# Kernel optimization log

Hardware: AMD Instinct MI355X
Metric: run time of the kernel (lower is better)

## Reference

```python
import jax, jax.numpy as jnp
import numpy as np

B, N, K, L = 16, 1024, 5, 3       # batch, atoms, kNN, egnn layers
D, M, H = 16, 64, 64              # embed_dim, m_dim, hidden_dim
EIN = 2 * D + 1                   # edge_mlp input: feats_i | feats_j | rel_dist
EPS, CLAMP = 1e-8, 2.0

def silu(x):
    return x * jax.nn.sigmoid(x)

def egnn_layer(feats, coors, mask, p):
    (eW1, eb1, eW2, eb2, gW, gb, cscale,
     cW1, cb1, cW2, cb2, nW1, nb1, nW2, nb2) = p
    b = feats.shape[0]
    rel_coors = coors[:, :, None, :] - coors[:, None, :, :]              # [B,N,N,3]
    rel_dist = jnp.sum(rel_coors ** 2, axis=-1)                          # [B,N,N] squared dist
    rank_mask = mask[:, :, None] & mask[:, None, :]
    ranking = jnp.where(rank_mask, rel_dist, 1e5)
    _, nbhd_idx = jax.lax.top_k(-ranking, K)                             # k nearest (incl self)
    rel_coors = jnp.take_along_axis(rel_coors, nbhd_idx[..., None], axis=2)   # [B,N,K,3]
    rel_dist = jnp.take_along_axis(rel_dist, nbhd_idx, axis=2)[..., None]     # [B,N,K,1]
    b_idx = jnp.arange(b)[:, None, None]
    feats_j = feats[b_idx, nbhd_idx]                                     # [B,N,K,D]
    feats_i = jnp.broadcast_to(feats[:, :, None, :], feats_j.shape)
    edge_in = jnp.concatenate([feats_i, feats_j, rel_dist], axis=-1)     # [B,N,K,2D+1]
    m_ij = silu(silu(edge_in @ eW1 + eb1) @ eW2 + eb2)                   # [B,N,K,M]
    m_ij = m_ij * jax.nn.sigmoid(m_ij @ gW + gb)                         # soft edge gate
    pair_mask = mask[:, :, None] & mask[b_idx, nbhd_idx]                 # [B,N,K]
    # coordinate update: CoorsNorm (unit vectors * learned scale) + clamped weights
    cw = (silu(m_ij @ cW1 + cb1) @ cW2 + cb2)[..., 0]                    # [B,N,K]
    sq = jnp.sum(rel_coors ** 2, axis=-1, keepdims=True)
    norm = jnp.sqrt(jnp.maximum(sq, EPS * EPS))                          # == norm.clamp(min=eps)
    rel_unit = rel_coors / norm * cscale
    cw = jnp.clip(jnp.where(pair_mask, cw, 0.0), -CLAMP, CLAMP)
    coors_out = jnp.einsum('bnk,bnkc->bnc', cw, rel_unit) + coors
    # node update: masked sum-pool of messages, residual MLP
    m_i = jnp.sum(jnp.where(pair_mask[..., None], m_ij, 0.0), axis=2)    # [B,N,M]
    node_in = jnp.concatenate([feats, m_i], axis=-1)
    feats_out = silu(node_in @ nW1 + nb1) @ nW2 + nb2 + feats
    return feats_out, coors_out

def _forward(atom_types, pos, mask, emb, eW1, eb1, eW2, eb2, gW, gb, cscale,
             cW1, cb1, cW2, cb2, nW1, nb1, nW2, nb2,
             hW1, hb1, hW2, hb2, hW3, hb3):
    maskf = mask.astype(jnp.float32)
    feats = emb[atom_types] * maskf[..., None]
    coors = pos * maskf[..., None]
    for l in range(L):
        p = (eW1[l], eb1[l], eW2[l], eb2[l], gW[l], gb[l], cscale[l],
             cW1[l], cb1[l], cW2[l], cb2[l], nW1[l], nb1[l], nW2[l], nb2[l])
        feats, coors = egnn_layer(feats, coors, mask, p)
    pooled = jnp.sum(feats * maskf[..., None], axis=1) / jnp.sum(maskf, axis=1, keepdims=True)
    x = jax.nn.relu(pooled @ hW1 + hb1)
    x = jax.nn.relu(x @ hW2 + hb2)
    return x @ hW3 + hb3                                                 # [B,1]

def setup_inputs():
    key = jax.random.key(0)
    ks = jax.random.split(key, 24)
    rn = lambda k, s, sc=0.05: jax.random.normal(k, s, jnp.float32) * sc
    return {
        "atom_types": jax.random.randint(ks[0], (B, N), 0, 6),
        "pos": jax.random.normal(ks[1], (B, N, 3), jnp.float32),
        "mask": jnp.ones((B, N), bool),
        "emb": rn(ks[2], (6, D), 1.0),
        "eW1": rn(ks[3], (L, EIN, 2 * EIN)), "eb1": rn(ks[4], (L, 2 * EIN)),
        "eW2": rn(ks[5], (L, 2 * EIN, M)), "eb2": rn(ks[6], (L, M)),
        "gW": rn(ks[7], (L, M, 1)), "gb": rn(ks[8], (L, 1)),
        "cscale": jnp.full((L, 1), 1e-2, jnp.float32),
        "cW1": rn(ks[9], (L, M, 4 * M)), "cb1": rn(ks[10], (L, 4 * M)),
        "cW2": rn(ks[11], (L, 4 * M, 1)), "cb2": rn(ks[12], (L, 1)),
        "nW1": rn(ks[13], (L, D + M, 2 * D)), "nb1": rn(ks[14], (L, 2 * D)),
        "nW2": rn(ks[15], (L, 2 * D, D)), "nb2": rn(ks[16], (L, D)),
        "hW1": rn(ks[17], (D, H)), "hb1": rn(ks[18], (H,)),
        "hW2": rn(ks[19], (H, H)), "hb2": rn(ks[20], (H,)),
        "hW3": rn(ks[21], (H, 1)), "hb3": rn(ks[22], (1,)),
    }

def reference(atom_types, pos, mask, emb, eW1, eb1, eW2, eb2, gW, gb, cscale,
              cW1, cb1, cW2, cb2, nW1, nb1, nW2, nb2,
              hW1, hb1, hW2, hb2, hW3, hb3):
    return _forward(atom_types, pos, mask, emb, eW1, eb1, eW2, eb2, gW, gb, cscale,
                    cW1, cb1, cW2, cb2, nW1, nb1, nW2, nb2,
                    hW1, hb1, hW2, hb2, hW3, hb3)
```

## Files before the change

### kernel.cpp

```cpp
#include <hip/hip_runtime.h>
#include <math.h>

#define BB    16
#define NPTS  1024
#define KNBR  5
#define NLAY  3
#define DIM   16
#define MDIM  64
#define HDIM  64

typedef short  bf16x8  __attribute__((ext_vector_type(8)));
typedef float  floatx4 __attribute__((ext_vector_type(4)));
union BU { uint4 u; bf16x8 s; };

__device__ __forceinline__ float sigf(float x){
  return __builtin_amdgcn_rcpf(1.0f + __expf(-x));
}
__device__ __forceinline__ float siluf(float x){ return x * sigf(x); }

__device__ __forceinline__ unsigned short f2bf(float x){
  float r;
  asm("v_cvt_pk_bf16_f32 %0, %1, %1" : "=v"(r) : "v"(x));
  return (unsigned short)(__float_as_uint(r) & 0xFFFFu);
}
__device__ __forceinline__ unsigned int f2bf2(float lo, float hi){
  float r;
  asm("v_cvt_pk_bf16_f32 %0, %1, %2" : "=v"(r) : "v"(lo), "v"(hi));
  return __float_as_uint(r);
}
__device__ __forceinline__ float bflo(unsigned int w){ return __uint_as_float(w<<16); }
__device__ __forceinline__ float bfhi(unsigned int w){ return __uint_as_float(w & 0xFFFF0000u); }

__global__ __launch_bounds__(256) void k_init(const int* __restrict__ types,
    const float* __restrict__ pos, const float* __restrict__ emb,
    float* __restrict__ feats, float* __restrict__ coorsS){
  int t = blockIdx.x*256 + threadIdx.x;
  if (t >= BB*NPTS) return;
  int a = types[t];
  #pragma unroll
  for (int d=0; d<DIM; ++d) feats[t*DIM+d] = emb[a*DIM+d];
  int b = t>>10, i = t&1023;
  coorsS[b*3072 + i]        = pos[t*3+0];
  coorsS[b*3072 + 1024 + i] = pos[t*3+1];
  coorsS[b*3072 + 2048 + i] = pos[t*3+2];
}

__global__ __launch_bounds__(256) void k_prep(const float* __restrict__ eW1,
    const float* __restrict__ eW2, const float* __restrict__ cW1,
    uint4* __restrict__ wf){
  int gid = blockIdx.x*256 + threadIdx.x;
  if (gid >= NLAY*3456) return;
  int l = gid / 3456;
  int r = gid - l*3456;
  unsigned short b[8];
  if (r < 640){
    int ct = r >> 7, kt = (r>>6)&1, lane = r&63;
    int k0 = kt*32 + (lane>>4)*8, col = ct*16 + (lane&15);
    #pragma unroll
    for (int j=0; j<8; ++j){
      int k = k0+j;
      float v = (k < 33 && col < 66) ? eW1[l*33*66 + k*66 + col] : 0.f;
      b[j] = f2bf(v);
    }
  } else if (r < 1408){
    int idx = r - 640;
    int ct = idx/192, kt = (idx>>6)%3, lane = idx&63;
    int k0 = kt*32 + (lane>>4)*8, col = ct*16 + (lane&15);
    #pragma unroll
    for (int j=0; j<8; ++j){
      int k = k0+j;
      float v = (k < 66) ? eW2[l*66*64 + k*64 + col] : 0.f;
      b[j] = f2bf(v);
    }
  } else {
    int idx = r - 1408;
    int lane = idx&63, t = idx>>6;
    int wb = t>>3, kt = (t>>2)&1, ct = t&3;
    int k0 = kt*32 + (lane>>4)*8, col = wb*64 + ct*16 + (lane&15);
    #pragma unroll
    for (int j=0; j<8; ++j)
      b[j] = f2bf(cW1[l*64*256 + (size_t)(k0+j)*256 + col]);
  }
  uint4 o;
  o.x = (unsigned)b[0] | ((unsigned)b[1]<<16);
  o.y = (unsigned)b[2] | ((unsigned)b[3]<<16);
  o.z = (unsigned)b[4] | ((unsigned)b[5]<<16);
  o.w = (unsigned)b[6] | ((unsigned)b[7]<<16);
  wf[gid] = o;
}

__global__ __launch_bounds__(256,4) void k_layer(
    const float* __restrict__ feats, const float* __restrict__ ciS,
    const uint4* __restrict__ wfL,
    const float* __restrict__ eb1, const float* __restrict__ eb2,
    const float* __restrict__ gW,  const float* __restrict__ gb,
    const float* __restrict__ cb1, const float* __restrict__ cW2,
    const float* __restrict__ cb2, const float* __restrict__ csc,
    const float* __restrict__ nW1, const float* __restrict__ nb1,
    const float* __restrict__ nW2, const float* __restrict__ nb2,
    float* __restrict__ feats_out, float* __restrict__ coS){

  __shared__ __align__(16) short sA[80*72];
  __shared__ __align__(16) short sB[80*104];
  __shared__ int nbr_l[80];
  float* smal = (float*)sB;
  float* redg = smal;
  float* gbuf = smal + 160;
  float* redc = smal + 240;
  float* cwl  = smal + 560;
  float* mind = smal + 640;
  float* hps  = smal + 1728;
  float* cxl = (float*)sB;
  float* cyl = cxl + 1024;
  float* czl = cxl + 2048;

  const int tid = threadIdx.x;
  const int n0  = blockIdx.x * 16;
  const int batch = n0 >> 10;
  const int bofs3 = batch * 3072;

  const uint4* bpW1 = wfL;
  const uint4* bpW2 = wfL + 640;
  const uint4* bpC  = wfL + 1408;

  {
    const float* cb = ciS + bofs3;
    #pragma unroll
    for (int t0=0; t0<4; ++t0){
      int t = tid + t0*256;
      cxl[t] = cb[t];
      cyl[t] = cb[1024+t];
      czl[t] = cb[2048+t];
    }
  }
  __syncthreads();

  const int wb = tid>>6, lane = tid&63;
  const int lr = lane&15, lh = lane>>4;

  {
#pragma clang fp contract(off)
    #pragma unroll 1
    for (int rr=0; rr<4; ++rr){
      int n = wb*4 + rr;
      int il = (n0 + n) & 1023;
      float xi = cxl[il], yi = cyl[il], zi = czl[il];
      float dist[16];
      #pragma unroll
      for (int t=0; t<16; ++t){
        int j = lane + (t<<6);
        float dx = xi - cxl[j];
        float dy = yi - cyl[j];
        float dz = zi - czl[j];
        float s = dx*dx; s += dy*dy; s += dz*dz;
        dist[t] = s;
      }
      #pragma unroll 1
      for (int r=0; r<KNBR; ++r){
        float g = dist[0];
        #pragma unroll
        for (int t=1; t<16; ++t) g = fminf(g, dist[t]);
        #pragma unroll
        for (int off=32; off>0; off>>=1) g = fminf(g, __shfl_xor(g, off));
        int bj = 0x7fffffff;
        #pragma unroll
        for (int t=15; t>=0; --t) if (dist[t]==g) bj = lane + (t<<6);
        #pragma unroll
        for (int off=32; off>0; off>>=1) bj = min(bj, __shfl_xor(bj, off));
        if (lane==0) nbr_l[n*KNBR + r] = bj;
        #pragma unroll
        for (int t=0; t<16; ++t) if (bj == lane + (t<<6)) dist[t] = 3.0e38f;
      }
    }
  }
  __syncthreads();

  if (tid < 160){
    int el = tid>>1, half = tid&1;
    int nl = el/5;
    int node_g = n0 + nl;
    int jl = nbr_l[el];
    int src = half ? ((batch<<10) + jl) : node_g;
    const float4* f4 = (const float4*)(feats + (size_t)src*DIM);
    float4 v0 = f4[0], v1 = f4[1], v2 = f4[2], v3 = f4[3];
    uint4 p0, p1;
    p0.x = f2bf2(v0.x, v0.y);
    p0.y = f2bf2(v0.z, v0.w);
    p0.z = f2bf2(v1.x, v1.y);
    p0.w = f2bf2(v1.z, v1.w);
    p1.x = f2bf2(v2.x, v2.y);
    p1.y = f2bf2(v2.z, v2.w);
    p1.z = f2bf2(v3.x, v3.y);
    p1.w = f2bf2(v3.z, v3.w);
    uint4* dst = (uint4*)(sA + el*72 + half*16);
    dst[0] = p0; dst[1] = p1;
    if (half == 0){
#pragma clang fp contract(off)
      int il = node_g & 1023;
      float ddx = cxl[il] - cxl[jl];
      float ddy = cyl[il] - cyl[jl];
      float ddz = czl[il] - czl[jl];
      float dist = ddx*ddx; dist += ddy*ddy; dist += ddz*ddz;
      uint4 z = {0,0,0,0};
      *(unsigned int*)(sA + el*72 + 32) = (unsigned)f2bf(dist);
      *(unsigned int*)(sA + el*72 + 34) = 0u;
      *(unsigned int*)(sA + el*72 + 36) = 0u;
      *(unsigned int*)(sA + el*72 + 38) = 0u;
      *(uint4*)(sA + el*72 + 40) = z;
      *(uint4*)(sA + el*72 + 48) = z;
      *(uint4*)(sA + el*72 + 56) = z;
    }
  }
  __syncthreads();

  {
    if (tid < 160){
      uint4 z = {0,0,0,0};
      int row = tid>>1, part = tid&1;
      *(uint4*)(sB + row*104 + 80 + part*8) = z;
    }
    #pragma unroll
    for (int rt=0; rt<5; ++rt){
      #pragma unroll
      for (int ct=0; ct<5; ++ct){
        if (((rt*5+ct)&3) == wb){
          bf16x8 a0 = *(const bf16x8*)(sA + (rt*16+lr)*72 + lh*8);
          bf16x8 a1 = *(const bf16x8*)(sA + (rt*16+lr)*72 + 32 + lh*8);
          BU b0, b1;
          b0.u = bpW1[ct*128 + lane];
          b1.u = bpW1[ct*128 + 64 + lane];
          floatx4 acc = (floatx4){0.f,0.f,0.f,0.f};
          acc = __builtin_amdgcn_mfma_f32_16x16x32_bf16(a0, b0.s, acc, 0,0,0);
          acc = __builtin_amdgcn_mfma_f32_16x16x32_bf16(a1, b1.s, acc, 0,0,0);
          int col = ct*16 + lr;
          float bias = (col < 66) ? eb1[col] : 0.f;
          #pragma unroll
          for (int reg=0; reg<4; ++reg){
            float v = (col < 66) ? siluf(acc[reg] + bias) : 0.f;
            sB[(rt*16 + lh*4 + reg)*104 + col] = (short)f2bf(v);
          }
        }
      }
    }
  }
  __syncthreads();

  {
    #pragma unroll
    for (int rt=0; rt<5; ++rt){
      floatx4 acc = (floatx4){0.f,0.f,0.f,0.f};
      #pragma unroll
      for (int kt=0; kt<3; ++kt){
        bf16x8 a = *(const bf16x8*)(sB + (rt*16+lr)*104 + kt*32 + lh*8);
        BU b; b.u = bpW2[wb*192 + kt*64 + lane];
        acc = __builtin_amdgcn_mfma_f32_16x16x32_bf16(a, b.s, acc, 0,0,0);
      }
      int col = wb*16 + lr;
      float bias = eb2[col];
      #pragma unroll
      for (int reg=0; reg<4; ++reg){
        float v = siluf(acc[reg] + bias);
        sA[(rt*16 + lh*4 + reg)*72 + col] = (short)f2bf(v);
      }
    }
  }
  __syncthreads();

  if (tid < 160){
    int e = tid>>1, half = tid&1;
    const uint4* mp = (const uint4*)(sA + e*72 + half*32);
    uint4 a = mp[0], b = mp[1], c = mp[2], d = mp[3];
    const float* gw = gW + half*32;
    float s;
    s  = bflo(a.x)*gw[0]  + bfhi(a.x)*gw[1]  + bflo(a.y)*gw[2]  + bfhi(a.y)*gw[3];
    s += bflo(a.z)*gw[4]  + bfhi(a.z)*gw[5]  + bflo(a.w)*gw[6]  + bfhi(a.w)*gw[7];
    s += bflo(b.x)*gw[8]  + bfhi(b.x)*gw[9]  + bflo(b.y)*gw[10] + bfhi(b.y)*gw[11];
    s += bflo(b.z)*gw[12] + bfhi(b.z)*gw[13] + bflo(b.w)*gw[14] + bfhi(b.w)*gw[15];
    s += bflo(c.x)*gw[16] + bfhi(c.x)*gw[17] + bflo(c.y)*gw[18] + bfhi(c.y)*gw[19];
    s += bflo(c.z)*gw[20] + bfhi(c.z)*gw[21] + bflo(c.w)*gw[22] + bfhi(c.w)*gw[23];
    s += bflo(d.x)*gw[24] + bfhi(d.x)*gw[25] + bflo(d.y)*gw[26] + bfhi(d.y)*gw[27];
    s += bflo(d.z)*gw[28] + bfhi(d.z)*gw[29] + bflo(d.w)*gw[30] + bfhi(d.w)*gw[31];
    redg[half*80 + e] = s;
  }
  __syncthreads();
  if (tid < 80) gbuf[tid] = sigf(redg[tid] + redg[80+tid] + gb[0]);
  __syncthreads();

  {
    float gv[5][4];
    #pragma unroll
    for (int rt=0; rt<5; ++rt)
      #pragma unroll
      for (int reg=0; reg<4; ++reg)
        gv[rt][reg] = gbuf[rt*16 + lh*4 + reg];
    float pacc[5][4];
    #pragma unroll
    for (int rt=0; rt<5; ++rt)
      #pragma unroll
      for (int reg=0; reg<4; ++reg) pacc[rt][reg] = 0.f;
    #pragma unroll
    for (int half=0; half<2; ++half){
      floatx4 acc[5][2];
      #pragma unroll
      for (int rt=0; rt<5; ++rt){
        acc[rt][0] = (floatx4){0.f,0.f,0.f,0.f};
        acc[rt][1] = (floatx4){0.f,0.f,0.f,0.f};
      }
      #pragma unroll
      for (int kt=0; kt<2; ++kt){
        bf16x8 av[5];
        #pragma unroll
        for (int rt=0; rt<5; ++rt)
          av[rt] = *(const bf16x8*)(sA + (rt*16+lr)*72 + kt*32 + lh*8);
        BU b0, b1;
        b0.u = bpC[((wb*2+kt)*4 + half*2 + 0)*64 + lane];
        b1.u = bpC[((wb*2+kt)*4 + half*2 + 1)*64 + lane];
        #pragma unroll
        for (int rt=0; rt<5; ++rt){
          acc[rt][0] = __builtin_amdgcn_mfma_f32_16x16x32_bf16(av[rt], b0.s, acc[rt][0], 0,0,0);
          acc[rt][1] = __builtin_amdgcn_mfma_f32_16x16x32_bf16(av[rt], b1.s, acc[rt][1], 0,0,0);
        }
      }
      #pragma unroll
      for (int c=0; c<2; ++c){
        int col = wb*64 + (half*2+c)*16 + lr;
        float b1v = cb1[col], w2v = cW2[col];
        #pragma unroll
        for (int rt=0; rt<5; ++rt){
          #pragma unroll
          for (int reg=0; reg<4; ++reg){
            pacc[rt][reg] += siluf(gv[rt][reg]*acc[rt][c][reg] + b1v) * w2v;
          }
        }
      }
    }
    #pragma unroll
    for (int rt=0; rt<5; ++rt){
      #pragma unroll
      for (int mask=1; mask<16; mask<<=1){
        #pragma unroll
        for (int reg=0; reg<4; ++reg)
          pacc[rt][reg] += __shfl_xor(pacc[rt][reg], mask);
      }
      if (lr == 0){
        #pragma unroll
        for (int reg=0; reg<4; ++reg)
          redc[wb*80 + rt*16 + lh*4 + reg] = pacc[rt][reg];
      }
    }
  }
  {
    int n = tid>>4, cq = tid&15;
    float g5[5];
    #pragma unroll
    for (int k=0; k<5; ++k) g5[k] = gbuf[n*5+k];
    float mi0=0.f, mi1=0.f, mi2=0.f, mi3=0.f;
    #pragma unroll
    for (int k=0; k<5; ++k){
      uint2 v = *(const uint2*)(sA + (n*5+k)*72 + cq*4);
      mi0 += g5[k]*bflo(v.x); mi1 += g5[k]*bfhi(v.x);
      mi2 += g5[k]*bflo(v.y); mi3 += g5[k]*bfhi(v.y);
    }
    float4 mv = {mi0, mi1, mi2, mi3};
    *(float4*)&mind[n*68 + cq*4] = mv;
  }
  __syncthreads();

  if (tid < 80)
    cwl[tid] = cb2[0] + redc[tid] + redc[80+tid] + redc[160+tid] + redc[240+tid];

  {
    int n = tid>>4, ot = tid&15;
    int node_g = n0 + n;
    const float* fb = feats + (size_t)node_g*DIM;
    float h0 = nb1[ot], h1 = nb1[ot+16];
    #pragma unroll
    for (int q=0; q<DIM; ++q){
      float x = fb[q];
      h0 += x*nW1[q*32+ot];
      h1 += x*nW1[q*32+ot+16];
    }
    #pragma unroll 8
    for (int c=0; c<64; ++c){
      float x = mind[n*68+c];
      h0 += x*nW1[(DIM+c)*32+ot];
      h1 += x*nW1[(DIM+c)*32+ot+16];
    }
    hps[n*32+ot]    = siluf(h0);
    hps[n*32+ot+16] = siluf(h1);
  }
  __syncthreads();

  {
    int n = tid>>4, d = tid&15;
    int node_g = n0 + n;
    float fo = nb2[d];
    #pragma unroll
    for (int o=0; o<32; ++o) fo += hps[n*32+o]*nW2[o*DIM+d];
    feats_out[(size_t)node_g*DIM + d] = fo + feats[(size_t)node_g*DIM + d];
  }

  if (tid < 16){
    int n = tid;
    int node_g = n0 + n;
    int il = node_g & 1023;
    float cs = csc[0];
    float cx = ciS[bofs3+il], cy = ciS[bofs3+1024+il], cz = ciS[bofs3+2048+il];
    float ax=0.f, ay=0.f, az=0.f;
    #pragma unroll
    for (int k=0; k<5; ++k){
      int jl = nbr_l[n*5 + k];
      float dx = cx - ciS[bofs3+jl];
      float dy = cy - ciS[bofs3+1024+jl];
      float dz = cz - ciS[bofs3+2048+jl];
      float sq = dx*dx + dy*dy + dz*dz;
      float inv = cs / sqrtf(fmaxf(sq, 1e-16f));
      float w = fminf(fmaxf(cwl[n*5+k], -2.f), 2.f);
      float wi = w*inv;
      ax += wi*dx; ay += wi*dy; az += wi*dz;
    }
    coS[bofs3+il]      = ax + cx;
    coS[bofs3+1024+il] = ay + cy;
    coS[bofs3+2048+il] = az + cz;
  }
}

__global__ __launch_bounds__(256) void k_head(const float* __restrict__ feats,
    const float* __restrict__ hW1, const float* __restrict__ hb1,
    const float* __restrict__ hW2, const float* __restrict__ hb2,
    const float* __restrict__ hW3, const float* __restrict__ hb3,
    float* __restrict__ out){
  int b = blockIdx.x, tid = threadIdx.x;
  __shared__ float red[256];
  __shared__ float pool[DIM];
  __shared__ float h1s[HDIM];
  __shared__ float h2s[HDIM];
  const float* fb = feats + (size_t)b*NPTS*DIM;
  int d = tid & 15, r0 = tid >> 4;
  float s = 0.f;
  for (int n=r0; n<NPTS; n+=16) s += fb[n*DIM+d];
  red[tid] = s;
  __syncthreads();
  if (tid < DIM){
    float t = 0.f;
    #pragma unroll
    for (int g=0; g<16; ++g) t += red[g*16+tid];
    pool[tid] = t * (1.0f/NPTS);
  }
  __syncthreads();
  if (tid < HDIM){
    float t = hb1[tid];
    #pragma unroll
    for (int q=0; q<DIM; ++q) t += pool[q]*hW1[q*HDIM+tid];
    h1s[tid] = fmaxf(t, 0.f);
  }
  __syncthreads();
  if (tid < HDIM){
    float t = hb2[tid];
    #pragma unroll
    for (int q=0; q<HDIM; ++q) t += h1s[q]*hW2[q*HDIM+tid];
    h2s[tid] = fmaxf(t, 0.f);
  }
  __syncthreads();
  if (tid == 0){
    float t = hb3[0];
    #pragma unroll
    for (int q=0; q<HDIM; ++q) t += h2s[q]*hW3[q];
    out[b] = t;
  }
}

extern "C" void kernel_launch(void* const* d_in, const int* in_sizes, int n_in,
                              void* d_out, int out_size, void* d_ws, size_t ws_size,
                              hipStream_t stream){
  const int*   types = (const int*)  d_in[0];
  const float* pos   = (const float*)d_in[1];
  const float* emb   = (const float*)d_in[3];
  const float* eW1   = (const float*)d_in[4];
  const float* eb1   = (const float*)d_in[5];
  const float* eW2   = (const float*)d_in[6];
  const float* eb2   = (const float*)d_in[7];
  const float* gW    = (const float*)d_in[8];
  const float* gb    = (const float*)d_in[9];
  const float* csc   = (const float*)d_in[10];
  const float* cW1   = (const float*)d_in[11];
  const float* cb1   = (const float*)d_in[12];
  const float* cW2   = (const float*)d_in[13];
  const float* cb2   = (const float*)d_in[14];
  const float* nW1   = (const float*)d_in[15];
  const float* nb1   = (const float*)d_in[16];
  const float* nW2   = (const float*)d_in[17];
  const float* nb2   = (const float*)d_in[18];
  const float* hW1   = (const float*)d_in[19];
  const float* hb1   = (const float*)d_in[20];
  const float* hW2   = (const float*)d_in[21];
  const float* hb2   = (const float*)d_in[22];
  const float* hW3   = (const float*)d_in[23];
  const float* hb3   = (const float*)d_in[24];
  float* out = (float*)d_out;

  float* ws     = (float*)d_ws;
  float* feats0 = ws;
  float* feats1 = feats0 + BB*NPTS*DIM;
  float* cS0    = feats1 + BB*NPTS*DIM;
  float* cS1    = cS0 + BB*3072;
  uint4* wf     = (uint4*)(cS1 + BB*3072);

  k_init<<<BB*NPTS/256, 256, 0, stream>>>(types, pos, emb, feats0, cS0);
  k_prep<<<(NLAY*3456+255)/256, 256, 0, stream>>>(eW1, eW2, cW1, wf);

  float* fi = feats0; float* fo_ = feats1;
  float* ci = cS0;    float* co  = cS1;
  for (int l=0; l<NLAY; ++l){
    k_layer<<<BB*NPTS/16, 256, 0, stream>>>(fi, ci, wf + l*3456,
        eb1 + l*66, eb2 + l*64, gW + l*64, gb + l,
        cb1 + l*256, cW2 + l*256, cb2 + l, csc + l,
        nW1 + l*80*32, nb1 + l*32, nW2 + l*32*16, nb2 + l*16,
        fo_, co);
    float* t = fi; fi = fo_; fo_ = t;
    t = ci; ci = co; co = t;
  }
  k_head<<<BB, 256, 0, stream>>>(fi, hW1, hb1, hW2, hb2, hW3, hb3, out);
}
```

Before: 254.1 us.

## Halve nodes per block, shrink LDS for higher occupancy, fuse setup kernels

Each layer block now handles 8 nodes (40 edges) instead of 16, doubling the grid. LDS is consolidated into one smaller buffer and launch bounds are raised to allow 8 blocks per CU. The kNN search now stores the selected squared distances so the edge-input build no longer recomputes them. The init and weight-prep kernels are merged into one launch. The trade-off is that the per-block coordinate load and the full 1024-point kNN scan are amortized over fewer nodes, and the MFMA tiles (3 row tiles for 40 rows) are partly padded.

```diff
diff --git a/kernel.cpp b/kernel.cpp
--- a/kernel.cpp
+++ b/kernel.cpp
@@ -6,8 +6,9 @@
 #define KNBR  5
 #define NLAY  3
 #define DIM   16
-#define MDIM  64
 #define HDIM  64
+#define NPB   8
+#define EDG   40
 
 typedef short  bf16x8  __attribute__((ext_vector_type(8)));
 typedef float  floatx4 __attribute__((ext_vector_type(4)));
@@ -31,24 +32,24 @@
 __device__ __forceinline__ float bflo(unsigned int w){ return __uint_as_float(w<<16); }
 __device__ __forceinline__ float bfhi(unsigned int w){ return __uint_as_float(w & 0xFFFF0000u); }
 
-__global__ __launch_bounds__(256) void k_init(const int* __restrict__ types,
+__global__ __launch_bounds__(256) void k_setup(const int* __restrict__ types,
     const float* __restrict__ pos, const float* __restrict__ emb,
-    float* __restrict__ feats, float* __restrict__ coorsS){
-  int t = blockIdx.x*256 + threadIdx.x;
-  if (t >= BB*NPTS) return;
-  int a = types[t];
-  #pragma unroll
-  for (int d=0; d<DIM; ++d) feats[t*DIM+d] = emb[a*DIM+d];
-  int b = t>>10, i = t&1023;
-  coorsS[b*3072 + i]        = pos[t*3+0];
-  coorsS[b*3072 + 1024 + i] = pos[t*3+1];
-  coorsS[b*3072 + 2048 + i] = pos[t*3+2];
-}
-
-__global__ __launch_bounds__(256) void k_prep(const float* __restrict__ eW1,
-    const float* __restrict__ eW2, const float* __restrict__ cW1,
+    const float* __restrict__ eW1, const float* __restrict__ eW2,
+    const float* __restrict__ cW1,
+    float* __restrict__ feats, float* __restrict__ coorsS,
     uint4* __restrict__ wf){
-  int gid = blockIdx.x*256 + threadIdx.x;
+  if (blockIdx.x < 64){
+    int t = blockIdx.x*256 + threadIdx.x;
+    int a = types[t];
+    #pragma unroll
+    for (int d=0; d<DIM; ++d) feats[t*DIM+d] = emb[a*DIM+d];
+    int b = t>>10, i = t&1023;
+    coorsS[b*3072 + i]        = pos[t*3+0];
+    coorsS[b*3072 + 1024 + i] = pos[t*3+1];
+    coorsS[b*3072 + 2048 + i] = pos[t*3+2];
+    return;
+  }
+  int gid = (blockIdx.x-64)*256 + threadIdx.x;
   if (gid >= NLAY*3456) return;
   int l = gid / 3456;
   int r = gid - l*3456;
@@ -89,7 +90,7 @@
   wf[gid] = o;
 }
 
-__global__ __launch_bounds__(256,4) void k_layer(
+__global__ __launch_bounds__(256,8) void k_layer(
     const float* __restrict__ feats, const float* __restrict__ ciS,
     const uint4* __restrict__ wfL,
     const float* __restrict__ eb1, const float* __restrict__ eb2,
@@ -100,22 +101,24 @@
     const float* __restrict__ nW2, const float* __restrict__ nb2,
     float* __restrict__ feats_out, float* __restrict__ coS){
 
-  __shared__ __align__(16) short sA[80*72];
-  __shared__ __align__(16) short sB[80*104];
-  __shared__ int nbr_l[80];
-  float* smal = (float*)sB;
+  __shared__ __align__(16) char lds_all[13056];
+  short* einA = (short*)lds_all;
+  short* h1A  = (short*)(lds_all + 5760);
+  float* cxl  = (float*)lds_all;
+  float* cyl  = cxl + 1024;
+  float* czl  = cxl + 2048;
+  int*   nbr_l  = (int*)(lds_all + 12736);
+  float* dist_l = (float*)(lds_all + 12896);
+  float* smal = (float*)(lds_all + 5760);
   float* redg = smal;
-  float* gbuf = smal + 160;
-  float* redc = smal + 240;
-  float* cwl  = smal + 560;
-  float* mind = smal + 640;
-  float* hps  = smal + 1728;
-  float* cxl = (float*)sB;
-  float* cyl = cxl + 1024;
-  float* czl = cxl + 2048;
+  float* gbuf = smal + 80;
+  float* redc = smal + 128;
+  float* cwl  = smal + 288;
+  float* mind = smal + 328;
+  float* hps  = smal + 872;
 
   const int tid = threadIdx.x;
-  const int n0  = blockIdx.x * 16;
+  const int n0  = blockIdx.x * NPB;
   const int batch = n0 >> 10;
   const int bofs3 = batch * 3072;
 
@@ -141,8 +144,8 @@
   {
 #pragma clang fp contract(off)
     #pragma unroll 1
-    for (int rr=0; rr<4; ++rr){
-      int n = wb*4 + rr;
+    for (int rr=0; rr<2; ++rr){
+      int n = wb*2 + rr;
       int il = (n0 + n) & 1023;
       float xi = cxl[il], yi = cyl[il], zi = czl[il];
       float dist[16];
@@ -167,7 +170,7 @@
         for (int t=15; t>=0; --t) if (dist[t]==g) bj = lane + (t<<6);
         #pragma unroll
         for (int off=32; off>0; off>>=1) bj = min(bj, __shfl_xor(bj, off));
-        if (lane==0) nbr_l[n*KNBR + r] = bj;
+        if (lane==0){ nbr_l[n*KNBR + r] = bj; dist_l[n*KNBR + r] = g; }
         #pragma unroll
         for (int t=0; t<16; ++t) if (bj == lane + (t<<6)) dist[t] = 3.0e38f;
       }
@@ -175,9 +178,9 @@
   }
   __syncthreads();
 
-  if (tid < 160){
+  if (tid < 2*EDG){
     int el = tid>>1, half = tid&1;
-    int nl = el/5;
+    int nl = el/KNBR;
     int node_g = n0 + nl;
     int jl = nbr_l[el];
     int src = half ? ((batch<<10) + jl) : node_g;
@@ -192,40 +195,30 @@
     p1.y = f2bf2(v2.z, v2.w);
     p1.z = f2bf2(v3.x, v3.y);
     p1.w = f2bf2(v3.z, v3.w);
-    uint4* dst = (uint4*)(sA + el*72 + half*16);
+    uint4* dst = (uint4*)(einA + el*72 + half*16);
     dst[0] = p0; dst[1] = p1;
     if (half == 0){
-#pragma clang fp contract(off)
-      int il = node_g & 1023;
-      float ddx = cxl[il] - cxl[jl];
-      float ddy = cyl[il] - cyl[jl];
-      float ddz = czl[il] - czl[jl];
-      float dist = ddx*ddx; dist += ddy*ddy; dist += ddz*ddz;
       uint4 z = {0,0,0,0};
-      *(unsigned int*)(sA + el*72 + 32) = (unsigned)f2bf(dist);
-      *(unsigned int*)(sA + el*72 + 34) = 0u;
-      *(unsigned int*)(sA + el*72 + 36) = 0u;
-      *(unsigned int*)(sA + el*72 + 38) = 0u;
-      *(uint4*)(sA + el*72 + 40) = z;
-      *(uint4*)(sA + el*72 + 48) = z;
-      *(uint4*)(sA + el*72 + 56) = z;
+      *(unsigned int*)(einA + el*72 + 32) = (unsigned)f2bf(dist_l[el]);
+      *(unsigned int*)(einA + el*72 + 34) = 0u;
+      *(unsigned int*)(einA + el*72 + 36) = 0u;
+      *(unsigned int*)(einA + el*72 + 38) = 0u;
+      *(uint4*)(einA + el*72 + 40) = z;
+      *(uint4*)(einA + el*72 + 48) = z;
+      *(uint4*)(einA + el*72 + 56) = z;
     }
   }
   __syncthreads();
 
   {
-    if (tid < 160){
-      uint4 z = {0,0,0,0};
-      int row = tid>>1, part = tid&1;
-      *(uint4*)(sB + row*104 + 80 + part*8) = z;
-    }
-    #pragma unroll
-    for (int rt=0; rt<5; ++rt){
+    if (tid < 36) ((unsigned int*)(h1A + 40*72))[tid] = 0u;
+    #pragma unroll
+    for (int rt=0; rt<3; ++rt){
       #pragma unroll
       for (int ct=0; ct<5; ++ct){
         if (((rt*5+ct)&3) == wb){
-          bf16x8 a0 = *(const bf16x8*)(sA + (rt*16+lr)*72 + lh*8);
-          bf16x8 a1 = *(const bf16x8*)(sA + (rt*16+lr)*72 + 32 + lh*8);
+          bf16x8 a0 = *(const bf16x8*)(einA + (rt*16+lr)*72 + lh*8);
+          bf16x8 a1 = *(const bf16x8*)(einA + (rt*16+lr)*72 + 32 + lh*8);
           BU b0, b1;
           b0.u = bpW1[ct*128 + lane];
           b1.u = bpW1[ct*128 + 64 + lane];
@@ -236,8 +229,10 @@
           float bias = (col < 66) ? eb1[col] : 0.f;
           #pragma unroll
           for (int reg=0; reg<4; ++reg){
+            int row = rt*16 + lh*4 + reg;
             float v = (col < 66) ? siluf(acc[reg] + bias) : 0.f;
-            sB[(rt*16 + lh*4 + reg)*104 + col] = (short)f2bf(v);
+            if (row < EDG && col < 72)
+              h1A[row*72 + col] = (short)f2bf(v);
           }
         }
       }
@@ -247,11 +242,11 @@
 
   {
     #pragma unroll
-    for (int rt=0; rt<5; ++rt){
+    for (int rt=0; rt<3; ++rt){
       floatx4 acc = (floatx4){0.f,0.f,0.f,0.f};
       #pragma unroll
       for (int kt=0; kt<3; ++kt){
-        bf16x8 a = *(const bf16x8*)(sB + (rt*16+lr)*104 + kt*32 + lh*8);
+        bf16x8 a = *(const bf16x8*)(h1A + (rt*16+lr)*72 + kt*32 + lh*8);
         BU b; b.u = bpW2[wb*192 + kt*64 + lane];
         acc = __builtin_amdgcn_mfma_f32_16x16x32_bf16(a, b.s, acc, 0,0,0);
       }
@@ -259,16 +254,18 @@
       float bias = eb2[col];
       #pragma unroll
       for (int reg=0; reg<4; ++reg){
+        int row = rt*16 + lh*4 + reg;
         float v = siluf(acc[reg] + bias);
-        sA[(rt*16 + lh*4 + reg)*72 + col] = (short)f2bf(v);
-      }
-    }
-  }
-  __syncthreads();
-
-  if (tid < 160){
+        if (row < EDG)
+          einA[row*72 + col] = (short)f2bf(v);
+      }
+    }
+  }
+  __syncthreads();
+
+  if (tid < 2*EDG){
     int e = tid>>1, half = tid&1;
-    const uint4* mp = (const uint4*)(sA + e*72 + half*32);
+    const uint4* mp = (const uint4*)(einA + e*72 + half*32);
     uint4 a = mp[0], b = mp[1], c = mp[2], d = mp[3];
     const float* gw = gW + half*32;
     float s;
@@ -280,43 +277,43 @@
     s += bflo(c.z)*gw[20] + bfhi(c.z)*gw[21] + bflo(c.w)*gw[22] + bfhi(c.w)*gw[23];
     s += bflo(d.x)*gw[24] + bfhi(d.x)*gw[25] + bflo(d.y)*gw[26] + bfhi(d.y)*gw[27];
     s += bflo(d.z)*gw[28] + bfhi(d.z)*gw[29] + bflo(d.w)*gw[30] + bfhi(d.w)*gw[31];
-    redg[half*80 + e] = s;
-  }
-  __syncthreads();
-  if (tid < 80) gbuf[tid] = sigf(redg[tid] + redg[80+tid] + gb[0]);
+    redg[half*EDG + e] = s;
+  }
+  __syncthreads();
+  if (tid < EDG) gbuf[tid] = sigf(redg[tid] + redg[EDG+tid] + gb[0]);
   __syncthreads();
 
   {
-    float gv[5][4];
-    #pragma unroll
-    for (int rt=0; rt<5; ++rt)
+    float gv[3][4];
+    #pragma unroll
+    for (int rt=0; rt<3; ++rt)
       #pragma unroll
       for (int reg=0; reg<4; ++reg)
         gv[rt][reg] = gbuf[rt*16 + lh*4 + reg];
-    float pacc[5][4];
-    #pragma unroll
-    for (int rt=0; rt<5; ++rt)
+    float pacc[3][4];
+    #pragma unroll
+    for (int rt=0; rt<3; ++rt)
       #pragma unroll
       for (int reg=0; reg<4; ++reg) pacc[rt][reg] = 0.f;
     #pragma unroll
     for (int half=0; half<2; ++half){
-      floatx4 acc[5][2];
-      #pragma unroll
-      for (int rt=0; rt<5; ++rt){
+      floatx4 acc[3][2];
+      #pragma unroll
+      for (int rt=0; rt<3; ++rt){
         acc[rt][0] = (floatx4){0.f,0.f,0.f,0.f};
         acc[rt][1] = (floatx4){0.f,0.f,0.f,0.f};
       }
       #pragma unroll
       for (int kt=0; kt<2; ++kt){
-        bf16x8 av[5];
-        #pragma unroll
-        for (int rt=0; rt<5; ++rt)
-          av[rt] = *(const bf16x8*)(sA + (rt*16+lr)*72 + kt*32 + lh*8);
+        bf16x8 av[3];
+        #pragma unroll
+        for (int rt=0; rt<3; ++rt)
+          av[rt] = *(const bf16x8*)(einA + (rt*16+lr)*72 + kt*32 + lh*8);
         BU b0, b1;
         b0.u = bpC[((wb*2+kt)*4 + half*2 + 0)*64 + lane];
         b1.u = bpC[((wb*2+kt)*4 + half*2 + 1)*64 + lane];
         #pragma unroll
-        for (int rt=0; rt<5; ++rt){
+        for (int rt=0; rt<3; ++rt){
           acc[rt][0] = __builtin_amdgcn_mfma_f32_16x16x32_bf16(av[rt], b0.s, acc[rt][0], 0,0,0);
           acc[rt][1] = __builtin_amdgcn_mfma_f32_16x16x32_bf16(av[rt], b1.s, acc[rt][1], 0,0,0);
         }
@@ -326,7 +323,7 @@
         int col = wb*64 + (half*2+c)*16 + lr;
         float b1v = cb1[col], w2v = cW2[col];
         #pragma unroll
-        for (int rt=0; rt<5; ++rt){
+        for (int rt=0; rt<3; ++rt){
           #pragma unroll
           for (int reg=0; reg<4; ++reg){
             pacc[rt][reg] += siluf(gv[rt][reg]*acc[rt][c][reg] + b1v) * w2v;
@@ -335,7 +332,7 @@
       }
     }
     #pragma unroll
-    for (int rt=0; rt<5; ++rt){
+    for (int rt=0; rt<3; ++rt){
       #pragma unroll
       for (int mask=1; mask<16; mask<<=1){
         #pragma unroll
@@ -344,20 +341,22 @@
       }
       if (lr == 0){
         #pragma unroll
-        for (int reg=0; reg<4; ++reg)
-          redc[wb*80 + rt*16 + lh*4 + reg] = pacc[rt][reg];
-      }
-    }
-  }
-  {
+        for (int reg=0; reg<4; ++reg){
+          int row = rt*16 + lh*4 + reg;
+          if (row < EDG) redc[wb*EDG + row] = pacc[rt][reg];
+        }
+      }
+    }
+  }
+  if (tid < NPB*16){
     int n = tid>>4, cq = tid&15;
-    float g5[5];
-    #pragma unroll
-    for (int k=0; k<5; ++k) g5[k] = gbuf[n*5+k];
+    float g5[KNBR];
+    #pragma unroll
+    for (int k=0; k<KNBR; ++k) g5[k] = gbuf[n*KNBR+k];
     float mi0=0.f, mi1=0.f, mi2=0.f, mi3=0.f;
     #pragma unroll
-    for (int k=0; k<5; ++k){
-      uint2 v = *(const uint2*)(sA + (n*5+k)*72 + cq*4);
+    for (int k=0; k<KNBR; ++k){
+      uint2 v = *(const uint2*)(einA + (n*KNBR+k)*72 + cq*4);
       mi0 += g5[k]*bflo(v.x); mi1 += g5[k]*bfhi(v.x);
       mi2 += g5[k]*bflo(v.y); mi3 += g5[k]*bfhi(v.y);
     }
@@ -366,10 +365,10 @@
   }
   __syncthreads();
 
-  if (tid < 80)
-    cwl[tid] = cb2[0] + redc[tid] + redc[80+tid] + redc[160+tid] + redc[240+tid];
-
-  {
+  if (tid < EDG)
+    cwl[tid] = cb2[0] + redc[tid] + redc[EDG+tid] + redc[2*EDG+tid] + redc[3*EDG+tid];
+
+  if (tid < NPB*16){
     int n = tid>>4, ot = tid&15;
     int node_g = n0 + n;
     const float* fb = feats + (size_t)node_g*DIM;
@@ -391,7 +390,7 @@
   }
   __syncthreads();
 
-  {
+  if (tid < NPB*16){
     int n = tid>>4, d = tid&15;
     int node_g = n0 + n;
     float fo = nb2[d];
@@ -400,7 +399,7 @@
     feats_out[(size_t)node_g*DIM + d] = fo + feats[(size_t)node_g*DIM + d];
   }
 
-  if (tid < 16){
+  if (tid < NPB){
     int n = tid;
     int node_g = n0 + n;
     int il = node_g & 1023;
@@ -408,14 +407,14 @@
     float cx = ciS[bofs3+il], cy = ciS[bofs3+1024+il], cz = ciS[bofs3+2048+il];
     float ax=0.f, ay=0.f, az=0.f;
     #pragma unroll
-    for (int k=0; k<5; ++k){
-      int jl = nbr_l[n*5 + k];
+    for (int k=0; k<KNBR; ++k){
+      int jl = nbr_l[n*KNBR + k];
       float dx = cx - ciS[bofs3+jl];
       float dy = cy - ciS[bofs3+1024+jl];
       float dz = cz - ciS[bofs3+2048+jl];
       float sq = dx*dx + dy*dy + dz*dz;
       float inv = cs / sqrtf(fmaxf(sq, 1e-16f));
-      float w = fminf(fmaxf(cwl[n*5+k], -2.f), 2.f);
+      float w = fminf(fmaxf(cwl[n*KNBR+k], -2.f), 2.f);
       float wi = w*inv;
       ax += wi*dx; ay += wi*dy; az += wi*dz;
     }
@@ -506,13 +505,13 @@
   float* cS1    = cS0 + BB*3072;
   uint4* wf     = (uint4*)(cS1 + BB*3072);
 
-  k_init<<<BB*NPTS/256, 256, 0, stream>>>(types, pos, emb, feats0, cS0);
-  k_prep<<<(NLAY*3456+255)/256, 256, 0, stream>>>(eW1, eW2, cW1, wf);
+  k_setup<<<64 + (NLAY*3456+255)/256, 256, 0, stream>>>(
+      types, pos, emb, eW1, eW2, cW1, feats0, cS0, wf);
 
   float* fi = feats0; float* fo_ = feats1;
   float* ci = cS0;    float* co  = cS1;
   for (int l=0; l<NLAY; ++l){
-    k_layer<<<BB*NPTS/16, 256, 0, stream>>>(fi, ci, wf + l*3456,
+    k_layer<<<BB*NPTS/NPB, 256, 0, stream>>>(fi, ci, wf + l*3456,
         eb1 + l*66, eb2 + l*64, gW + l*64, gb + l,
         cb1 + l*256, cW2 + l*256, cb2 + l, csc + l,
         nW1 + l*80*32, nb1 + l*32, nW2 + l*32*16, nb2 + l*16,
```

After: 364.5 us. 43.4% more time.
